# Kernel tuning notes

Measured on AMD Instinct MI355X. Metric: run time of the kernel, lower is better.

Reference implementation:

```python
import jax, jax.numpy as jnp
import numpy as np

BN_EPS = 1e-3  # keras BatchNormalization default epsilon


def setup_inputs() -> dict:
    key = jax.random.key(0)
    ks = jax.random.split(key, 8)
    B, F, Df = 256, 64, 256   # batch, num_features, feature_dim
    E, H, D = 8, 256, 256     # num_experts, hidden, expert_dim
    s1 = 1.0 / np.sqrt(Df)
    s2 = 1.0 / np.sqrt(H)
    return {
        "x":  jax.random.normal(ks[0], (B, F, Df), jnp.float32),
        "Wr": jax.random.normal(ks[1], (Df, E), jnp.float32) * s1,
        "br": jnp.zeros((E,), jnp.float32),
        "W1": jax.random.normal(ks[2], (E, Df, H), jnp.float32) * s1,
        "b1": jnp.zeros((E, H), jnp.float32),
        "g1": jnp.ones((E, H), jnp.float32),
        "be1": jnp.zeros((E, H), jnp.float32),
        "m1": jnp.zeros((E, H), jnp.float32),
        "v1": jnp.ones((E, H), jnp.float32),
        "W2": jax.random.normal(ks[3], (E, H, H), jnp.float32) * s2,
        "b2": jnp.zeros((E, H), jnp.float32),
        "g2": jnp.ones((E, H), jnp.float32),
        "be2": jnp.zeros((E, H), jnp.float32),
        "m2": jnp.zeros((E, H), jnp.float32),
        "v2": jnp.ones((E, H), jnp.float32),
        "Wo": jax.random.normal(ks[4], (E, H, D), jnp.float32) * s2,
        "bo": jnp.zeros((E, D), jnp.float32),
    }


def _bn(h, g, b, m, v):
    # inference-mode batch norm with moving stats; params are [E,H], h is [B,F,E,H]
    return g * (h - m) * jax.lax.rsqrt(v + BN_EPS) + b


def reference(x, Wr, br, W1, b1, g1, be1, m1, v1,
              W2, b2, g2, be2, m2, v2, Wo, bo):
    # learned softmax routing: mean over batch -> [F, Df] -> dense -> softmax
    feat = jnp.mean(x, axis=0)                     # [F, Df]
    w = jax.nn.softmax(feat @ Wr + br, axis=-1)    # [F, E]

    # all experts at once: Dense -> BN -> relu, x2, then Dense output
    h = jnp.einsum('bfd,edh->bfeh', x, W1) + b1    # [B, F, E, H]
    h = jax.nn.relu(_bn(h, g1, be1, m1, v1))
    h = jnp.einsum('bfeh,ehk->bfek', h, W2) + b2
    h = jax.nn.relu(_bn(h, g2, be2, m2, v2))
    y = jnp.einsum('bfeh,ehd->bfed', h, Wo) + bo   # [B, F, E, D]

    # weighted combine over experts (routing weights broadcast over batch)
    return jnp.einsum('bfed,fe->bfd', y, w)        # [B, F, D]
```

## Files before the change

kernel.cpp:

```cpp
#include <hip/hip_runtime.h>
#include <hip/hip_bf16.h>
#include <stdint.h>

#define BN_EPS 1e-3f

typedef __bf16 bf16x8 __attribute__((ext_vector_type(8)));
typedef float  f32x16 __attribute__((ext_vector_type(16)));

static constexpr size_t WS_FOLD_OFF = 24ull * 131072ull;
static constexpr size_t WS_WRT_OFF  = WS_FOLD_OFF + 32768ull;
static constexpr size_t WS_WB_OFF   = WS_WRT_OFF + 2048ull;

__global__ __launch_bounds__(256) void fold_kernel(
    const float* __restrict__ b1, const float* __restrict__ g1, const float* __restrict__ be1,
    const float* __restrict__ m1, const float* __restrict__ v1,
    const float* __restrict__ b2, const float* __restrict__ g2, const float* __restrict__ be2,
    const float* __restrict__ m2, const float* __restrict__ v2,
    float* __restrict__ fold) {
  int i = blockIdx.x * 256 + threadIdx.x;
  if (i < 2048) {
    float s1 = g1[i] * rsqrtf(v1[i] + BN_EPS);
    fold[i]        = s1;
    fold[2048 + i] = (b1[i] - m1[i]) * s1 + be1[i];
    float s2 = g2[i] * rsqrtf(v2[i] + BN_EPS);
    fold[4096 + i] = s2;
    fold[6144 + i] = (b2[i] - m2[i]) * s2 + be2[i];
  }
}

__global__ __launch_bounds__(256) void pack_kernel(
    const float* __restrict__ W1, const float* __restrict__ W2, const float* __restrict__ Wo,
    __bf16* __restrict__ pk) {
  __shared__ float sl[16 * 256];
  int bid = blockIdx.x;
  int m = bid >> 4, ks = bid & 15;
  int L = m >> 3, e = m & 7;
  const float* Ws = (L == 0 ? W1 : (L == 1 ? W2 : Wo)) + (size_t)e * 65536 + (size_t)ks * 16 * 256;
  int t = threadIdx.x;
#pragma unroll
  for (int it = 0; it < 4; ++it) {
    int el4 = it * 256 + t;
    float4 v = *reinterpret_cast<const float4*>(Ws + (size_t)el4 * 4);
    *reinterpret_cast<float4*>(&sl[el4 * 4]) = v;
  }
  __syncthreads();
#pragma unroll
  for (int it = 0; it < 2; ++it) {
    int task = it * 256 + t;
    int nb = task >> 6, l = task & 63;
    int colb = nb * 32 + (l & 31);
    int krow = (l >> 5) * 8;
    union { __bf16 h[8]; int4 v; } u;
#pragma unroll
    for (int i = 0; i < 8; ++i) u.h[i] = (__bf16)sl[(krow + i) * 256 + colb];
    size_t off = ((size_t)(m * 8 + nb) * 16 + ks) * 512 + (size_t)l * 8;
    *reinterpret_cast<int4*>(pk + off) = u.v;
  }
}

__global__ __launch_bounds__(256) void route_kernel(
    const float* __restrict__ x, const float* __restrict__ Wr, const float* __restrict__ br,
    const float* __restrict__ bo, float* __restrict__ wrt, float* __restrict__ wb) {
  __shared__ float4 part[4][64];
  __shared__ float feat[256];
  __shared__ float lg[8];
  __shared__ float wsm[8];
  int f = blockIdx.x, t = threadIdx.x;
  int bq = t >> 6, dq = t & 63;
  float4 s = {0.f, 0.f, 0.f, 0.f};
  const float* xp = x + (size_t)(bq * 64) * 16384 + f * 256 + dq * 4;
  for (int bi = 0; bi < 64; ++bi) {
    float4 v = *reinterpret_cast<const float4*>(xp + (size_t)bi * 16384);
    s.x += v.x; s.y += v.y; s.z += v.z; s.w += v.w;
  }
  part[bq][dq] = s;
  __syncthreads();
  if (t < 64) {
    float4 a = part[0][t], b = part[1][t], c = part[2][t], d = part[3][t];
    float4 r;
    r.x = (a.x + b.x) + (c.x + d.x); r.y = (a.y + b.y) + (c.y + d.y);
    r.z = (a.z + b.z) + (c.z + d.z); r.w = (a.w + b.w) + (c.w + d.w);
    r.x *= (1.f/256.f); r.y *= (1.f/256.f); r.z *= (1.f/256.f); r.w *= (1.f/256.f);
    *reinterpret_cast<float4*>(&feat[t * 4]) = r;
  }
  __syncthreads();
  if (t < 8) {
    float a = br[t];
    for (int d = 0; d < 256; ++d) a += feat[d] * Wr[d * 8 + t];
    lg[t] = a;
  }
  __syncthreads();
  if (t == 0) {
    float mx = lg[0];
#pragma unroll
    for (int e = 1; e < 8; ++e) mx = fmaxf(mx, lg[e]);
    float ex[8]; float sum = 0.f;
#pragma unroll
    for (int e = 0; e < 8; ++e) { ex[e] = expf(lg[e] - mx); sum += ex[e]; }
    float inv = 1.0f / sum;
#pragma unroll
    for (int e = 0; e < 8; ++e) { float v = ex[e] * inv; wsm[e] = v; wrt[f * 8 + e] = v; }
  }
  __syncthreads();
  float o = 0.f;
#pragma unroll
  for (int e = 0; e < 8; ++e) o += wsm[e] * bo[e * 256 + t];
  wb[f * 256 + t] = o;
}

__device__ __forceinline__ void phase_swapped(
    const char* __restrict__ src, char* __restrict__ dst,
    const __bf16* __restrict__ pb, const float* __restrict__ sA, const float* __restrict__ cA,
    int l, int l31, int hi, int w) {
  f32x16 acc[4];
#pragma unroll
  for (int mt = 0; mt < 4; ++mt)
#pragma unroll
    for (int r = 0; r < 16; ++r) acc[mt][r] = 0.f;
  bf16x8 bq = *reinterpret_cast<const bf16x8*>(pb + (size_t)l * 8);
#pragma unroll
  for (int ks = 0; ks < 16; ++ks) {
    bf16x8 bn = (ks < 15) ? *reinterpret_cast<const bf16x8*>(pb + (size_t)(ks + 1) * 512 + (size_t)l * 8) : bq;
#pragma unroll
    for (int mt = 0; mt < 4; ++mt) {
      bf16x8 xf = *reinterpret_cast<const bf16x8*>(src + (((2 * ks + hi) * 128 + mt * 32 + l31) << 4));
      acc[mt] = __builtin_amdgcn_mfma_f32_32x32x16_bf16(bq, xf, acc[mt], 0, 0, 0);
    }
    bq = bn;
  }
  __syncthreads();
#pragma unroll
  for (int g = 0; g < 4; ++g) {
    float4 s4 = *reinterpret_cast<const float4*>(sA + 8 * g);
    float4 c4 = *reinterpret_cast<const float4*>(cA + 8 * g);
#pragma unroll
    for (int mt = 0; mt < 4; ++mt) {
      union { __bf16 h[4]; uint2 u; } p;
#pragma unroll
      for (int j = 0; j < 4; ++j) {
        float sj = (&s4.x)[j], cj = (&c4.x)[j];
        p.h[j] = (__bf16)fmaxf(acc[mt][4 * g + j] * sj + cj, 0.f);
      }
      int addr = (((w * 4 + g) * 128 + mt * 32 + l31) << 4) + hi * 8;
      *reinterpret_cast<uint2*>(dst + addr) = p.u;
    }
  }
  __syncthreads();
}

__global__ __launch_bounds__(512, 2) void moe_kernel(
    const float* __restrict__ x, const __bf16* __restrict__ pk,
    const float* __restrict__ fold, const float* __restrict__ wrt,
    const float* __restrict__ wb, float* __restrict__ out) {
  __shared__ char xb[65536];
  __shared__ char hb[65536];
  __shared__ float wrts[512];
  const int tid = threadIdx.x;
  const int l = tid & 63, w = tid >> 6;
  const int l31 = l & 31, hi = l >> 5;
  const int bid = blockIdx.x;
  const int tile = bid >> 1, eh = bid & 1;

  {
    const float* xg = x + (size_t)tile * 32768;
    int tok = w * 16 + (l & 15);
    int kc = l >> 4;
#pragma unroll
    for (int i = 0; i < 8; ++i) {
      int fr = kc * 8 + i;
      const float* src = xg + (size_t)tok * 256 + fr * 8;
      float4 v0 = *reinterpret_cast<const float4*>(src);
      float4 v1 = *reinterpret_cast<const float4*>(src + 4);
      union { __bf16 h[8]; int4 v; } u;
      u.h[0] = (__bf16)v0.x; u.h[1] = (__bf16)v0.y; u.h[2] = (__bf16)v0.z; u.h[3] = (__bf16)v0.w;
      u.h[4] = (__bf16)v1.x; u.h[5] = (__bf16)v1.y; u.h[6] = (__bf16)v1.z; u.h[7] = (__bf16)v1.w;
      *reinterpret_cast<int4*>(xb + ((fr * 128 + tok) << 4)) = u.v;
    }
  }
  if (tid < 512) wrts[tid] = wrt[tid];

  f32x16 outacc[4];
#pragma unroll
  for (int mt = 0; mt < 4; ++mt)
#pragma unroll
    for (int r = 0; r < 16; ++r) outacc[mt][r] = 0.f;

  __syncthreads();

#pragma unroll 1
  for (int ep = 0; ep < 4; ++ep) {
    const int e = eh * 4 + ep;
    phase_swapped(xb, hb, pk + (size_t)((0 * 8 + e) * 8 + w) * 8192,
                  fold + 0 * 4096 + e * 256 + w * 32 + 4 * hi,
                  fold + 0 * 4096 + 2048 + e * 256 + w * 32 + 4 * hi, l, l31, hi, w);
    phase_swapped(hb, hb, pk + (size_t)((1 * 8 + e) * 8 + w) * 8192,
                  fold + 1 * 4096 + e * 256 + w * 32 + 4 * hi,
                  fold + 1 * 4096 + 2048 + e * 256 + w * 32 + 4 * hi, l, l31, hi, w);
    {
      f32x16 acc[4];
#pragma unroll
      for (int mt = 0; mt < 4; ++mt)
#pragma unroll
        for (int r = 0; r < 16; ++r) acc[mt][r] = 0.f;
      const __bf16* pb = pk + (size_t)((2 * 8 + e) * 8 + w) * 8192;
      bf16x8 bq = *reinterpret_cast<const bf16x8*>(pb + (size_t)l * 8);
#pragma unroll
      for (int ks = 0; ks < 16; ++ks) {
        bf16x8 bn = (ks < 15) ? *reinterpret_cast<const bf16x8*>(pb + (size_t)(ks + 1) * 512 + (size_t)l * 8) : bq;
#pragma unroll
        for (int mt = 0; mt < 4; ++mt) {
          bf16x8 hf = *reinterpret_cast<const bf16x8*>(hb + (((2 * ks + hi) * 128 + mt * 32 + l31) << 4));
          acc[mt] = __builtin_amdgcn_mfma_f32_32x32x16_bf16(hf, bq, acc[mt], 0, 0, 0);
        }
        bq = bn;
      }
#pragma unroll
      for (int mt = 0; mt < 4; ++mt) {
#pragma unroll
        for (int r = 0; r < 16; ++r) {
          int row = mt * 32 + 4 * hi + (r & 3) + 8 * (r >> 2);
          outacc[mt][r] += wrts[(row & 63) * 8 + e] * acc[mt][r];
        }
      }
    }
  }

  float* og = out + (size_t)tile * 32768;
  const int col = w * 32 + l31;
#pragma unroll
  for (int mt = 0; mt < 4; ++mt) {
#pragma unroll
    for (int r = 0; r < 16; ++r) {
      int row = mt * 32 + 4 * hi + (r & 3) + 8 * (r >> 2);
      float v = outacc[mt][r];
      if (eh == 0) v += wb[(row & 63) * 256 + col];
      unsafeAtomicAdd(og + row * 256 + col, v);
    }
  }
}

extern "C" void kernel_launch(void* const* d_in, const int* in_sizes, int n_in,
                              void* d_out, int out_size, void* d_ws, size_t ws_size,
                              hipStream_t stream) {
  const float* x   = (const float*)d_in[0];
  const float* Wr  = (const float*)d_in[1];
  const float* br  = (const float*)d_in[2];
  const float* W1  = (const float*)d_in[3];
  const float* b1  = (const float*)d_in[4];
  const float* g1  = (const float*)d_in[5];
  const float* be1 = (const float*)d_in[6];
  const float* m1  = (const float*)d_in[7];
  const float* v1  = (const float*)d_in[8];
  const float* W2  = (const float*)d_in[9];
  const float* b2  = (const float*)d_in[10];
  const float* g2  = (const float*)d_in[11];
  const float* be2 = (const float*)d_in[12];
  const float* m2  = (const float*)d_in[13];
  const float* v2  = (const float*)d_in[14];
  const float* Wo  = (const float*)d_in[15];
  const float* bo  = (const float*)d_in[16];
  float* out = (float*)d_out;

  __bf16* pk  = (__bf16*)d_ws;
  float* fold = (float*)((char*)d_ws + WS_FOLD_OFF);
  float* wrt  = (float*)((char*)d_ws + WS_WRT_OFF);
  float* wb   = (float*)((char*)d_ws + WS_WB_OFF);

  hipMemsetAsync(out, 0, (size_t)out_size * sizeof(float), stream);
  hipLaunchKernelGGL(fold_kernel, dim3(8), dim3(256), 0, stream,
                     b1, g1, be1, m1, v1, b2, g2, be2, m2, v2, fold);
  hipLaunchKernelGGL(pack_kernel, dim3(384), dim3(256), 0, stream, W1, W2, Wo, pk);
  hipLaunchKernelGGL(route_kernel, dim3(64), dim3(256), 0, stream, x, Wr, br, bo, wrt, wb);
  hipLaunchKernelGGL(moe_kernel, dim3(256), dim3(512), 0, stream, x, pk, fold, wrt, wb, out);
}
```

Baseline: 115.9 us.

## Halve MoE token tile, add XOR LDS swizzle, split routing reduction

The token tile per block drops from 128 to 64 rows, so the grid doubles to 512 blocks and LDS per block halves, allowing 4 blocks per CU by launch bounds. LDS addressing gains an XOR swizzle to cut bank conflicts on MFMA operand loads. Routing is split into a parallel partial-sum kernel across 8 batch chunks plus a finishing kernel. The partial sums are written to workspace space that the pack kernel later overwrites, which depends on launch ordering. The cost is twice as many weight reads per token, since each weight tile is reused over fewer tokens.

```diff
diff --git a/kernel.cpp b/kernel.cpp
--- a/kernel.cpp
+++ b/kernel.cpp
@@ -10,6 +10,8 @@
 static constexpr size_t WS_FOLD_OFF = 24ull * 131072ull;
 static constexpr size_t WS_WRT_OFF  = WS_FOLD_OFF + 32768ull;
 static constexpr size_t WS_WB_OFF   = WS_WRT_OFF + 2048ull;
+
+#define XADDR(fr, tok) (((fr) << 10) + ((((tok) ^ (fr))) << 4))
 
 __global__ __launch_bounds__(256) void fold_kernel(
     const float* __restrict__ b1, const float* __restrict__ g1, const float* __restrict__ be1,
@@ -58,36 +60,32 @@
   }
 }
 
-__global__ __launch_bounds__(256) void route_kernel(
-    const float* __restrict__ x, const float* __restrict__ Wr, const float* __restrict__ br,
+__global__ __launch_bounds__(256) void route1_kernel(
+    const float* __restrict__ x, float* __restrict__ part) {
+  int f = blockIdx.x, bq = blockIdx.y, t = threadIdx.x;
+  const float* xp = x + (size_t)(bq * 32) * 16384 + f * 256 + t;
+  float s = 0.f;
+#pragma unroll 4
+  for (int bi = 0; bi < 32; ++bi) s += xp[(size_t)bi * 16384];
+  part[(size_t)(bq * 64 + f) * 256 + t] = s;
+}
+
+__global__ __launch_bounds__(256) void route2_kernel(
+    const float* __restrict__ part, const float* __restrict__ Wr, const float* __restrict__ br,
     const float* __restrict__ bo, float* __restrict__ wrt, float* __restrict__ wb) {
-  __shared__ float4 part[4][64];
   __shared__ float feat[256];
   __shared__ float lg[8];
   __shared__ float wsm[8];
   int f = blockIdx.x, t = threadIdx.x;
-  int bq = t >> 6, dq = t & 63;
-  float4 s = {0.f, 0.f, 0.f, 0.f};
-  const float* xp = x + (size_t)(bq * 64) * 16384 + f * 256 + dq * 4;
-  for (int bi = 0; bi < 64; ++bi) {
-    float4 v = *reinterpret_cast<const float4*>(xp + (size_t)bi * 16384);
-    s.x += v.x; s.y += v.y; s.z += v.z; s.w += v.w;
-  }
-  part[bq][dq] = s;
-  __syncthreads();
-  if (t < 64) {
-    float4 a = part[0][t], b = part[1][t], c = part[2][t], d = part[3][t];
-    float4 r;
-    r.x = (a.x + b.x) + (c.x + d.x); r.y = (a.y + b.y) + (c.y + d.y);
-    r.z = (a.z + b.z) + (c.z + d.z); r.w = (a.w + b.w) + (c.w + d.w);
-    r.x *= (1.f/256.f); r.y *= (1.f/256.f); r.z *= (1.f/256.f); r.w *= (1.f/256.f);
-    *reinterpret_cast<float4*>(&feat[t * 4]) = r;
-  }
+  float a = 0.f;
+#pragma unroll
+  for (int bq = 0; bq < 8; ++bq) a += part[(size_t)(bq * 64 + f) * 256 + t];
+  feat[t] = a * (1.0f / 256.0f);
   __syncthreads();
   if (t < 8) {
-    float a = br[t];
-    for (int d = 0; d < 256; ++d) a += feat[d] * Wr[d * 8 + t];
-    lg[t] = a;
+    float s = br[t];
+    for (int d = 0; d < 256; ++d) s += feat[d] * Wr[d * 8 + t];
+    lg[t] = s;
   }
   __syncthreads();
   if (t == 0) {
@@ -108,52 +106,58 @@
   wb[f * 256 + t] = o;
 }
 
-__device__ __forceinline__ void phase_swapped(
-    const char* __restrict__ src, char* __restrict__ dst,
-    const __bf16* __restrict__ pb, const float* __restrict__ sA, const float* __restrict__ cA,
-    int l, int l31, int hi, int w) {
-  f32x16 acc[4];
-#pragma unroll
-  for (int mt = 0; mt < 4; ++mt)
+__device__ __forceinline__ void sweep(
+    const char* __restrict__ src, const __bf16* __restrict__ pb,
+    int l, int l31, int hi, int swap, f32x16 acc[2]) {
+#pragma unroll
+  for (int mt = 0; mt < 2; ++mt)
 #pragma unroll
     for (int r = 0; r < 16; ++r) acc[mt][r] = 0.f;
   bf16x8 bq = *reinterpret_cast<const bf16x8*>(pb + (size_t)l * 8);
 #pragma unroll
   for (int ks = 0; ks < 16; ++ks) {
     bf16x8 bn = (ks < 15) ? *reinterpret_cast<const bf16x8*>(pb + (size_t)(ks + 1) * 512 + (size_t)l * 8) : bq;
-#pragma unroll
-    for (int mt = 0; mt < 4; ++mt) {
-      bf16x8 xf = *reinterpret_cast<const bf16x8*>(src + (((2 * ks + hi) * 128 + mt * 32 + l31) << 4));
-      acc[mt] = __builtin_amdgcn_mfma_f32_32x32x16_bf16(bq, xf, acc[mt], 0, 0, 0);
+    int fr = 2 * ks + hi;
+    bf16x8 a0 = *reinterpret_cast<const bf16x8*>(src + XADDR(fr, l31));
+    bf16x8 a1 = *reinterpret_cast<const bf16x8*>(src + XADDR(fr, 32 + l31));
+    if (swap) {
+      acc[0] = __builtin_amdgcn_mfma_f32_32x32x16_bf16(bq, a0, acc[0], 0, 0, 0);
+      acc[1] = __builtin_amdgcn_mfma_f32_32x32x16_bf16(bq, a1, acc[1], 0, 0, 0);
+    } else {
+      acc[0] = __builtin_amdgcn_mfma_f32_32x32x16_bf16(a0, bq, acc[0], 0, 0, 0);
+      acc[1] = __builtin_amdgcn_mfma_f32_32x32x16_bf16(a1, bq, acc[1], 0, 0, 0);
     }
     bq = bn;
   }
-  __syncthreads();
+}
+
+__device__ __forceinline__ void epi_store(
+    const f32x16 acc[2], const float* __restrict__ sA, const float* __restrict__ cA,
+    char* __restrict__ dst, int l31, int hi, int w) {
 #pragma unroll
   for (int g = 0; g < 4; ++g) {
     float4 s4 = *reinterpret_cast<const float4*>(sA + 8 * g);
     float4 c4 = *reinterpret_cast<const float4*>(cA + 8 * g);
-#pragma unroll
-    for (int mt = 0; mt < 4; ++mt) {
+    int fr = w * 4 + g;
+#pragma unroll
+    for (int mt = 0; mt < 2; ++mt) {
       union { __bf16 h[4]; uint2 u; } p;
 #pragma unroll
       for (int j = 0; j < 4; ++j) {
         float sj = (&s4.x)[j], cj = (&c4.x)[j];
         p.h[j] = (__bf16)fmaxf(acc[mt][4 * g + j] * sj + cj, 0.f);
       }
-      int addr = (((w * 4 + g) * 128 + mt * 32 + l31) << 4) + hi * 8;
-      *reinterpret_cast<uint2*>(dst + addr) = p.u;
-    }
-  }
-  __syncthreads();
-}
-
-__global__ __launch_bounds__(512, 2) void moe_kernel(
+      *reinterpret_cast<uint2*>(dst + XADDR(fr, mt * 32 + l31) + hi * 8) = p.u;
+    }
+  }
+}
+
+__global__ __launch_bounds__(512, 4) void moe_kernel(
     const float* __restrict__ x, const __bf16* __restrict__ pk,
     const float* __restrict__ fold, const float* __restrict__ wrt,
     const float* __restrict__ wb, float* __restrict__ out) {
-  __shared__ char xb[65536];
-  __shared__ char hb[65536];
+  __shared__ char xb[32768];
+  __shared__ char hb[32768];
   __shared__ float wrts[512];
   const int tid = threadIdx.x;
   const int l = tid & 63, w = tid >> 6;
@@ -162,78 +166,64 @@
   const int tile = bid >> 1, eh = bid & 1;
 
   {
-    const float* xg = x + (size_t)tile * 32768;
-    int tok = w * 16 + (l & 15);
-    int kc = l >> 4;
-#pragma unroll
-    for (int i = 0; i < 8; ++i) {
-      int fr = kc * 8 + i;
-      const float* src = xg + (size_t)tok * 256 + fr * 8;
+    const float* xg = x + (size_t)tile * 16384;
+#pragma unroll
+    for (int i = 0; i < 4; ++i) {
+      int u = i * 512 + tid;
+      int tok = u >> 5, k8 = u & 31;
+      const float* src = xg + (size_t)tok * 256 + k8 * 8;
       float4 v0 = *reinterpret_cast<const float4*>(src);
       float4 v1 = *reinterpret_cast<const float4*>(src + 4);
-      union { __bf16 h[8]; int4 v; } u;
-      u.h[0] = (__bf16)v0.x; u.h[1] = (__bf16)v0.y; u.h[2] = (__bf16)v0.z; u.h[3] = (__bf16)v0.w;
-      u.h[4] = (__bf16)v1.x; u.h[5] = (__bf16)v1.y; u.h[6] = (__bf16)v1.z; u.h[7] = (__bf16)v1.w;
-      *reinterpret_cast<int4*>(xb + ((fr * 128 + tok) << 4)) = u.v;
-    }
-  }
-  if (tid < 512) wrts[tid] = wrt[tid];
-
-  f32x16 outacc[4];
-#pragma unroll
-  for (int mt = 0; mt < 4; ++mt)
+      union { __bf16 h[8]; int4 v; } p;
+      p.h[0] = (__bf16)v0.x; p.h[1] = (__bf16)v0.y; p.h[2] = (__bf16)v0.z; p.h[3] = (__bf16)v0.w;
+      p.h[4] = (__bf16)v1.x; p.h[5] = (__bf16)v1.y; p.h[6] = (__bf16)v1.z; p.h[7] = (__bf16)v1.w;
+      *reinterpret_cast<int4*>(xb + XADDR(k8, tok)) = p.v;
+    }
+  }
+  wrts[tid] = wrt[tid];
+
+  f32x16 outacc[2];
+#pragma unroll
+  for (int mt = 0; mt < 2; ++mt)
 #pragma unroll
     for (int r = 0; r < 16; ++r) outacc[mt][r] = 0.f;
 
   __syncthreads();
 
+  f32x16 acc[2];
 #pragma unroll 1
   for (int ep = 0; ep < 4; ++ep) {
     const int e = eh * 4 + ep;
-    phase_swapped(xb, hb, pk + (size_t)((0 * 8 + e) * 8 + w) * 8192,
-                  fold + 0 * 4096 + e * 256 + w * 32 + 4 * hi,
-                  fold + 0 * 4096 + 2048 + e * 256 + w * 32 + 4 * hi, l, l31, hi, w);
-    phase_swapped(hb, hb, pk + (size_t)((1 * 8 + e) * 8 + w) * 8192,
-                  fold + 1 * 4096 + e * 256 + w * 32 + 4 * hi,
-                  fold + 1 * 4096 + 2048 + e * 256 + w * 32 + 4 * hi, l, l31, hi, w);
-    {
-      f32x16 acc[4];
-#pragma unroll
-      for (int mt = 0; mt < 4; ++mt)
-#pragma unroll
-        for (int r = 0; r < 16; ++r) acc[mt][r] = 0.f;
-      const __bf16* pb = pk + (size_t)((2 * 8 + e) * 8 + w) * 8192;
-      bf16x8 bq = *reinterpret_cast<const bf16x8*>(pb + (size_t)l * 8);
-#pragma unroll
-      for (int ks = 0; ks < 16; ++ks) {
-        bf16x8 bn = (ks < 15) ? *reinterpret_cast<const bf16x8*>(pb + (size_t)(ks + 1) * 512 + (size_t)l * 8) : bq;
-#pragma unroll
-        for (int mt = 0; mt < 4; ++mt) {
-          bf16x8 hf = *reinterpret_cast<const bf16x8*>(hb + (((2 * ks + hi) * 128 + mt * 32 + l31) << 4));
-          acc[mt] = __builtin_amdgcn_mfma_f32_32x32x16_bf16(hf, bq, acc[mt], 0, 0, 0);
-        }
-        bq = bn;
+    sweep(xb, pk + (size_t)((0 * 8 + e) * 8 + w) * 8192, l, l31, hi, 1, acc);
+    __syncthreads();
+    epi_store(acc, fold + 0 * 4096 + e * 256 + w * 32 + 4 * hi,
+              fold + 0 * 4096 + 2048 + e * 256 + w * 32 + 4 * hi, hb, l31, hi, w);
+    __syncthreads();
+    sweep(hb, pk + (size_t)((1 * 8 + e) * 8 + w) * 8192, l, l31, hi, 1, acc);
+    __syncthreads();
+    epi_store(acc, fold + 1 * 4096 + e * 256 + w * 32 + 4 * hi,
+              fold + 1 * 4096 + 2048 + e * 256 + w * 32 + 4 * hi, hb, l31, hi, w);
+    __syncthreads();
+    sweep(hb, pk + (size_t)((2 * 8 + e) * 8 + w) * 8192, l, l31, hi, 0, acc);
+#pragma unroll
+    for (int mt = 0; mt < 2; ++mt) {
+#pragma unroll
+      for (int r = 0; r < 16; ++r) {
+        int row = mt * 32 + 4 * hi + (r & 3) + 8 * (r >> 2);
+        outacc[mt][r] += wrts[row * 8 + e] * acc[mt][r];
       }
-#pragma unroll
-      for (int mt = 0; mt < 4; ++mt) {
-#pragma unroll
-        for (int r = 0; r < 16; ++r) {
-          int row = mt * 32 + 4 * hi + (r & 3) + 8 * (r >> 2);
-          outacc[mt][r] += wrts[(row & 63) * 8 + e] * acc[mt][r];
-        }
-      }
-    }
-  }
-
-  float* og = out + (size_t)tile * 32768;
+    }
+  }
+
+  float* og = out + (size_t)tile * 16384;
   const int col = w * 32 + l31;
 #pragma unroll
-  for (int mt = 0; mt < 4; ++mt) {
+  for (int mt = 0; mt < 2; ++mt) {
 #pragma unroll
     for (int r = 0; r < 16; ++r) {
       int row = mt * 32 + 4 * hi + (r & 3) + 8 * (r >> 2);
       float v = outacc[mt][r];
-      if (eh == 0) v += wb[(row & 63) * 256 + col];
+      if (eh == 0) v += wb[row * 256 + col];
       unsafeAtomicAdd(og + row * 256 + col, v);
     }
   }
@@ -262,14 +252,16 @@
   float* out = (float*)d_out;
 
   __bf16* pk  = (__bf16*)d_ws;
+  float* part = (float*)d_ws;
   float* fold = (float*)((char*)d_ws + WS_FOLD_OFF);
   float* wrt  = (float*)((char*)d_ws + WS_WRT_OFF);
   float* wb   = (float*)((char*)d_ws + WS_WB_OFF);
 
   hipMemsetAsync(out, 0, (size_t)out_size * sizeof(float), stream);
+  hipLaunchKernelGGL(route1_kernel, dim3(64, 8), dim3(256), 0, stream, x, part);
+  hipLaunchKernelGGL(route2_kernel, dim3(64), dim3(256), 0, stream, part, Wr, br, bo, wrt, wb);
   hipLaunchKernelGGL(fold_kernel, dim3(8), dim3(256), 0, stream,
                      b1, g1, be1, m1, v1, b2, g2, be2, m2, v2, fold);
   hipLaunchKernelGGL(pack_kernel, dim3(384), dim3(256), 0, stream, W1, W2, Wo, pk);
-  hipLaunchKernelGGL(route_kernel, dim3(64), dim3(256), 0, stream, x, Wr, br, bo, wrt, wb);
-  hipLaunchKernelGGL(moe_kernel, dim3(256), dim3(512), 0, stream, x, pk, fold, wrt, wb, out);
-}
+  hipLaunchKernelGGL(moe_kernel, dim3(512), dim3(512), 0, stream, x, pk, fold, wrt, wb, out);
+}
```

Result: slower. 127.1 us (+9.6%).
